# Performance work log

Hardware: AMD Instinct MI355X
Metric: run time of the kernel (lower is better)

The kernel has to match this reference:

```python
import jax, jax.numpy as jnp
import numpy as np

B, Q, H, W = 64, 300, 40, 40  # batch, num_queries, feature-map H,W (img/32)


def setup_inputs() -> dict:
    key = jax.random.key(0)
    k1, k2, k3 = jax.random.split(key, 3)
    obj_coord = jax.random.uniform(k1, (B, Q, 4), dtype=jnp.float32)  # sigmoid cxcywh
    sub_coord = jax.random.uniform(k2, (B, Q, 4), dtype=jnp.float32)
    img_size = jax.random.randint(k3, (B, 2), 800, 1280, dtype=jnp.int64)  # (h, w)
    mask = jnp.zeros((B, H, W), dtype=bool)  # only its shape is used
    return {"obj_coord": obj_coord, "sub_coord": sub_coord, "img_size": img_size, "mask": mask}


def _box_cxcywh_to_xyxy(b):
    cx, cy, w, h = b[..., 0], b[..., 1], b[..., 2], b[..., 3]
    return cx - 0.5 * w, cy - 0.5 * h, cx + 0.5 * w, cy + 0.5 * h


def _mask_from_query(coord, img_size, Hm, Wm):
    # coord: [B,Q,4] cxcywh in [0,1]; img_size: [B,2] = (img_h, img_w)
    x1, y1, x2, y2 = _box_cxcywh_to_xyxy(coord)
    sw = img_size[:, 1:2].astype(jnp.float32)  # [B,1]
    sh = img_size[:, 0:1].astype(jnp.float32)
    # torch: (coord * size) // 32 then .long()  (floor division on floats == floor)
    x1 = jnp.floor(x1 * sw / 32.0).astype(jnp.int32)
    y1 = jnp.floor(y1 * sh / 32.0).astype(jnp.int32)
    x2 = jnp.floor(x2 * sw / 32.0).astype(jnp.int32)
    y2 = jnp.floor(y2 * sh / 32.0).astype(jnp.int32)
    x2 = jnp.minimum(x2, Wm - 1)
    y2 = jnp.minimum(y2, Hm - 1)
    hh = jnp.arange(Hm, dtype=jnp.int32)[:, None]  # [H,1]
    ww = jnp.arange(Wm, dtype=jnp.int32)[None, :]  # [1,W]
    # True OUTSIDE the (inclusive) box: single fused broadcast compare, [B,Q,H,W]
    return ((hh < y1[..., None, None]) | (hh > y2[..., None, None]) |
            (ww < x1[..., None, None]) | (ww > x2[..., None, None]))


def reference(obj_coord, sub_coord, img_size, mask):
    Hm, Wm = mask.shape[1], mask.shape[2]
    mask_object = _mask_from_query(obj_coord, img_size, Hm, Wm)
    mask_human = _mask_from_query(sub_coord, img_size, Hm, Wm)
    # stack object/human masks; float32 so fwd and fwdbwd share output structure
    return jnp.stack([mask_object, mask_human], axis=0).astype(jnp.float32)
```

## Files before the change

kernel.cpp:

```cpp
#include <hip/hip_runtime.h>
#include <stdint.h>


#define B_ 64
#define Q_ 300
#define HM 40
#define WM 40
#define NBOX (2 * B_ * Q_)
#define N4   15360000

__global__ __launch_bounds__(256) void box_prep_kernel(
    const float* __restrict__ obj,
    const float* __restrict__ sub,
    const int*   __restrict__ img,
    uint32_t*    __restrict__ tbl)
{
    #pragma clang fp contract(off)
    int id = blockIdx.x * 256 + threadIdx.x;
    if (id >= NBOX) return;

    int q  = id % Q_;
    int sb = id / Q_;
    int b  = sb & 63;
    int s  = sb >> 6;

    const float* coord = s ? sub : obj;
    float4 c = ((const float4*)coord)[b * Q_ + q];

    float sh = (float)img[b * 2 + 0];
    float sw = (float)img[b * 2 + 1];

    float x1f = (c.x - 0.5f * c.z) * sw / 32.0f;
    float y1f = (c.y - 0.5f * c.w) * sh / 32.0f;
    float x2f = (c.x + 0.5f * c.z) * sw / 32.0f;
    float y2f = (c.y + 0.5f * c.w) * sh / 32.0f;

    int x1 = (int)floorf(x1f);
    int y1 = (int)floorf(y1f);
    int x2 = min((int)floorf(x2f), WM - 1);
    int y2 = min((int)floorf(y2f), HM - 1);

    uint64_t lo = (x1 <= 0) ? ~0ull : ~((1ull << x1) - 1ull);
    uint64_t hi = (1ull << (x2 + 1)) - 1ull;
    uint64_t outside = (~(lo & hi)) & ((1ull << 40) - 1ull);

    uint32_t d0 = (uint32_t)outside;
    uint32_t d1 = ((uint32_t)(outside >> 32) & 0xFFu)
                | (((uint32_t)y1 & 0xFFu) << 8)
                | (((uint32_t)y2 & 0xFFu) << 16);

    tbl[id * 2 + 0] = d0;
    tbl[id * 2 + 1] = d1;
}

__global__ __launch_bounds__(256) void partmap_stream_kernel(
    const uint32_t* __restrict__ tbl,
    float4*         __restrict__ out)
{
    int idx = blockIdx.x * 256 + threadIdx.x;

    int sbq = idx / 400;
    int rem = idx - sbq * 400;
    int h   = rem / 10;
    int w4  = rem - h * 10;

    uint32_t d0 = tbl[sbq * 2 + 0];
    uint32_t d1 = tbl[sbq * 2 + 1];

    int y1 = (int)(int8_t)(d1 >> 8);
    int y2 = (int)(int8_t)(d1 >> 16);

    int rneg = ((h - y1) | (y2 - h)) >> 31;

    int w0 = w4 * 4;
    uint32_t shifted = (uint32_t)((((uint64_t)d1 << 32) | d0) >> w0);
    uint32_t m = shifted | (uint32_t)rneg;

    float4 r;
    r.x = (float)( m        & 1u);
    r.y = (float)((m >> 1)  & 1u);
    r.z = (float)((m >> 2)  & 1u);
    r.w = (float)((m >> 3)  & 1u);

    out[idx] = r;
}

extern "C" void kernel_launch(void* const* d_in, const int* in_sizes, int n_in,
                              void* d_out, int out_size, void* d_ws, size_t ws_size,
                              hipStream_t stream) {
    const float* obj = (const float*)d_in[0];
    const float* sub = (const float*)d_in[1];
    const int*   img = (const int*)d_in[2];

    uint32_t* tbl = (uint32_t*)d_ws;
    float4*   out = (float4*)d_out;

    box_prep_kernel<<<dim3((NBOX + 255) / 256), dim3(256), 0, stream>>>(obj, sub, img, tbl);
    partmap_stream_kernel<<<dim3(N4 / 256), dim3(256), 0, stream>>>(tbl, out);
}
```

Baseline: 234.7 us.

## Fuse box prep into streaming kernel with per-block shared box table

Merges the two kernels into one: each 256-thread block computes 16 box descriptors into shared memory, synchronises, then loops to write those maps' 6400 float4 outputs using nontemporal stores. This removes the second launch, the global table round-trip and the per-thread division by 400. The cost is a serial prep phase on 16 threads plus a barrier in every block, and a 25-iteration store loop per thread instead of one store per thread.

```diff
diff --git a/kernel.cpp b/kernel.cpp
--- a/kernel.cpp
+++ b/kernel.cpp
@@ -7,82 +7,89 @@
 #define HM 40
 #define WM 40
 #define NBOX (2 * B_ * Q_)
-#define N4   15360000
+#define MAPS_PER_BLOCK 16
+#define NBLOCKS (NBOX / MAPS_PER_BLOCK)
+#define F4_PER_MAP 400
+#define ITERS ((MAPS_PER_BLOCK * F4_PER_MAP) / 256)
 
-__global__ __launch_bounds__(256) void box_prep_kernel(
+typedef float vfloat4 __attribute__((ext_vector_type(4)));
+
+__global__ __launch_bounds__(256) void partmap_fused_kernel(
     const float* __restrict__ obj,
     const float* __restrict__ sub,
     const int*   __restrict__ img,
-    uint32_t*    __restrict__ tbl)
+    vfloat4*     __restrict__ out)
 {
-    #pragma clang fp contract(off)
-    int id = blockIdx.x * 256 + threadIdx.x;
-    if (id >= NBOX) return;
+    __shared__ uint32_t s_d0[MAPS_PER_BLOCK];
+    __shared__ uint32_t s_d1[MAPS_PER_BLOCK];
 
-    int q  = id % Q_;
-    int sb = id / Q_;
-    int b  = sb & 63;
-    int s  = sb >> 6;
+    const int tid = threadIdx.x;
 
-    const float* coord = s ? sub : obj;
-    float4 c = ((const float4*)coord)[b * Q_ + q];
+    if (tid < MAPS_PER_BLOCK) {
+        #pragma clang fp contract(off)
+        int id = blockIdx.x * MAPS_PER_BLOCK + tid;
+        int q  = id % Q_;
+        int sb = id / Q_;
+        int b  = sb & 63;
+        int s  = sb >> 6;
 
-    float sh = (float)img[b * 2 + 0];
-    float sw = (float)img[b * 2 + 1];
+        const float* coord = s ? sub : obj;
+        float4 c = ((const float4*)coord)[b * Q_ + q];
 
-    float x1f = (c.x - 0.5f * c.z) * sw / 32.0f;
-    float y1f = (c.y - 0.5f * c.w) * sh / 32.0f;
-    float x2f = (c.x + 0.5f * c.z) * sw / 32.0f;
-    float y2f = (c.y + 0.5f * c.w) * sh / 32.0f;
+        float sh = (float)img[b * 2 + 0];
+        float sw = (float)img[b * 2 + 1];
 
-    int x1 = (int)floorf(x1f);
-    int y1 = (int)floorf(y1f);
-    int x2 = min((int)floorf(x2f), WM - 1);
-    int y2 = min((int)floorf(y2f), HM - 1);
+        float x1f = (c.x - 0.5f * c.z) * sw / 32.0f;
+        float y1f = (c.y - 0.5f * c.w) * sh / 32.0f;
+        float x2f = (c.x + 0.5f * c.z) * sw / 32.0f;
+        float y2f = (c.y + 0.5f * c.w) * sh / 32.0f;
 
-    uint64_t lo = (x1 <= 0) ? ~0ull : ~((1ull << x1) - 1ull);
-    uint64_t hi = (1ull << (x2 + 1)) - 1ull;
-    uint64_t outside = (~(lo & hi)) & ((1ull << 40) - 1ull);
+        int x1 = (int)floorf(x1f);
+        int y1 = (int)floorf(y1f);
+        int x2 = min((int)floorf(x2f), WM - 1);
+        int y2 = min((int)floorf(y2f), HM - 1);
 
-    uint32_t d0 = (uint32_t)outside;
-    uint32_t d1 = ((uint32_t)(outside >> 32) & 0xFFu)
-                | (((uint32_t)y1 & 0xFFu) << 8)
-                | (((uint32_t)y2 & 0xFFu) << 16);
+        uint64_t lo = (x1 <= 0) ? ~0ull : ~((1ull << x1) - 1ull);
+        uint64_t hi = (1ull << (x2 + 1)) - 1ull;
+        uint64_t outside = (~(lo & hi)) & ((1ull << 40) - 1ull);
 
-    tbl[id * 2 + 0] = d0;
-    tbl[id * 2 + 1] = d1;
-}
+        s_d0[tid] = (uint32_t)outside;
+        s_d1[tid] = ((uint32_t)(outside >> 32) & 0xFFu)
+                  | (((uint32_t)y1 & 0xFFu) << 8)
+                  | (((uint32_t)y2 & 0xFFu) << 16);
+    }
+    __syncthreads();
 
-__global__ __launch_bounds__(256) void partmap_stream_kernel(
-    const uint32_t* __restrict__ tbl,
-    float4*         __restrict__ out)
-{
-    int idx = blockIdx.x * 256 + threadIdx.x;
+    int rem = tid;
+    int lm  = 0;
+    vfloat4* __restrict__ p = out + (size_t)blockIdx.x * (MAPS_PER_BLOCK * F4_PER_MAP) + tid;
 
-    int sbq = idx / 400;
-    int rem = idx - sbq * 400;
-    int h   = rem / 10;
-    int w4  = rem - h * 10;
+    for (int it = 0; it < ITERS; ++it) {
+        uint32_t d0 = s_d0[lm];
+        uint32_t d1 = s_d1[lm];
 
-    uint32_t d0 = tbl[sbq * 2 + 0];
-    uint32_t d1 = tbl[sbq * 2 + 1];
+        int h  = rem / 10;
+        int w0 = (rem - h * 10) * 4;
 
-    int y1 = (int)(int8_t)(d1 >> 8);
-    int y2 = (int)(int8_t)(d1 >> 16);
+        int y1 = (int)(int8_t)(d1 >> 8);
+        int y2 = (int)(int8_t)(d1 >> 16);
 
-    int rneg = ((h - y1) | (y2 - h)) >> 31;
+        int rneg = ((h - y1) | (y2 - h)) >> 31;
 
-    int w0 = w4 * 4;
-    uint32_t shifted = (uint32_t)((((uint64_t)d1 << 32) | d0) >> w0);
-    uint32_t m = shifted | (uint32_t)rneg;
+        uint32_t m = (uint32_t)((((uint64_t)d1 << 32) | d0) >> w0) | (uint32_t)rneg;
 
-    float4 r;
-    r.x = (float)( m        & 1u);
-    r.y = (float)((m >> 1)  & 1u);
-    r.z = (float)((m >> 2)  & 1u);
-    r.w = (float)((m >> 3)  & 1u);
+        vfloat4 r;
+        r.x = (float)( m        & 1u);
+        r.y = (float)((m >> 1)  & 1u);
+        r.z = (float)((m >> 2)  & 1u);
+        r.w = (float)((m >> 3)  & 1u);
 
-    out[idx] = r;
+        __builtin_nontemporal_store(r, p);
+
+        rem += 256;
+        if (rem >= F4_PER_MAP) { rem -= F4_PER_MAP; ++lm; }
+        p += 256;
+    }
 }
 
 extern "C" void kernel_launch(void* const* d_in, const int* in_sizes, int n_in,
@@ -91,10 +98,8 @@
     const float* obj = (const float*)d_in[0];
     const float* sub = (const float*)d_in[1];
     const int*   img = (const int*)d_in[2];
+    (void)d_ws; (void)ws_size;
 
-    uint32_t* tbl = (uint32_t*)d_ws;
-    float4*   out = (float4*)d_out;
-
-    box_prep_kernel<<<dim3((NBOX + 255) / 256), dim3(256), 0, stream>>>(obj, sub, img, tbl);
-    partmap_stream_kernel<<<dim3(N4 / 256), dim3(256), 0, stream>>>(tbl, out);
+    partmap_fused_kernel<<<dim3(NBLOCKS), dim3(256), 0, stream>>>(
+        obj, sub, img, (vfloat4*)d_out);
 }
```

Result: slower. 252.0 us (+7.4%).
